# Kernel tuning notes

Hardware: AMD Instinct MI355X
Metric: run time of the kernel (lower is better)

The kernel has to match this reference:

```python
import jax, jax.numpy as jnp
import numpy as np

D_MODEL = 1024
N_HEADS = 16
D_HEAD = D_MODEL // N_HEADS
D_FF = 4096
ALPHA = 2.0
EPS = 1e-5


def _layernorm(x, g, b):
    mu = jnp.mean(x, axis=-1, keepdims=True)
    var = jnp.mean(jnp.square(x - mu), axis=-1, keepdims=True)
    return (x - mu) * jax.lax.rsqrt(var + EPS) * g + b


def _mish(x):
    return x * jnp.tanh(jax.nn.softplus(x))


def setup_inputs() -> dict:
    key = jax.random.key(0)
    ks = jax.random.split(key, 10)
    s = 1.0 / np.sqrt(D_MODEL)
    sf = 1.0 / np.sqrt(D_FF)
    return {
        "x": jax.random.normal(ks[0], (2, 2048, D_MODEL), jnp.float32),
        "Wq": jax.random.normal(ks[1], (D_MODEL, D_MODEL), jnp.float32) * s,
        "Wk": jax.random.normal(ks[2], (D_MODEL, D_MODEL), jnp.float32) * s,
        "Wv": jax.random.normal(ks[3], (D_MODEL, D_MODEL), jnp.float32) * s,
        "Wo": jax.random.normal(ks[4], (D_MODEL, D_MODEL), jnp.float32) * s,
        "W1": jax.random.normal(ks[5], (D_MODEL, D_FF), jnp.float32) * s,
        "b1": jnp.zeros((D_FF,), jnp.float32),
        "W2": jax.random.normal(ks[6], (D_FF, D_MODEL), jnp.float32) * sf,
        "b2": jnp.zeros((D_MODEL,), jnp.float32),
        "g1": jnp.ones((D_MODEL,), jnp.float32),
        "be1": jnp.zeros((D_MODEL,), jnp.float32),
        "g2": jnp.ones((D_MODEL,), jnp.float32),
        "be2": jnp.zeros((D_MODEL,), jnp.float32),
    }


def reference(x, Wq, Wk, Wv, Wo, W1, b1, W2, b2, g1, be1, g2, be2):
    B, T, C = x.shape
    # --- multi-head self-attention (no mask, eval-mode dropout) ---
    def split_heads(t):  # [B,T,C] -> [B,H,T,Dh]
        return t.reshape(B, T, N_HEADS, D_HEAD).transpose(0, 2, 1, 3)
    Q = split_heads(x @ Wq)
    K = split_heads(x @ Wk)
    V = split_heads(x @ Wv)
    scale = 1.0 / np.sqrt(D_HEAD).astype(np.float32)
    attn = jnp.einsum('bhqd,bhkd->bhqk', Q, K) * scale
    attn = jax.nn.softmax(attn, axis=-1)
    ctx = jnp.einsum('bhqk,bhkd->bhqd', attn, V)
    ctx = ctx.transpose(0, 2, 1, 3).reshape(B, T, C)
    attn_out = ctx @ Wo
    # --- DeepNorm residual 1 ---
    x = _layernorm(ALPHA * x + attn_out, g1, be1)
    # --- feed-forward (Mish) ---
    h = _mish(x @ W1 + b1)
    ff_out = h @ W2 + b2
    # --- DeepNorm residual 2 ---
    return _layernorm(ALPHA * x + ff_out, g2, be2)
```

## Files before the change

kernel.cpp:

```cpp
#include <hip/hip_runtime.h>
#include <hip/hip_bf16.h>

typedef unsigned short u16;
typedef unsigned int   u32;
typedef __attribute__((ext_vector_type(8))) short  short8;
typedef __attribute__((ext_vector_type(4))) short  short4v;
typedef __attribute__((ext_vector_type(4))) float  f32x4;

static __device__ __forceinline__ u16 f2bf(float f) {
  u32 u = __builtin_bit_cast(u32, f);
  u = (u + 0x7fffu + ((u >> 16) & 1u)) >> 16;
  return (u16)u;
}

#define MFMA_16x16x32(A,B,C) __builtin_amdgcn_mfma_f32_16x16x32_bf16((A),(B),(C),0,0,0)

static __device__ __forceinline__ void gload_lds16(const u16* g, u16* lds) {
  __builtin_amdgcn_global_load_lds((const __attribute__((address_space(1))) u32*)g,
                                   (__attribute__((address_space(3))) u32*)lds, 16, 0, 0);
}

static __device__ __forceinline__ float mishf(float x) {
  float sp = fmaxf(x, 0.f) + log1pf(__expf(-fabsf(x)));
  return x * tanhf(sp);
}

__global__ __launch_bounds__(256) void cast_bf16_kernel(const float* __restrict__ x,
                                                        u16* __restrict__ o) {
  int i = (blockIdx.x * 256 + threadIdx.x) * 4;
  float4 v = *(const float4*)&x[i];
  short4v s;
  s[0] = (short)f2bf(v.x); s[1] = (short)f2bf(v.y);
  s[2] = (short)f2bf(v.z); s[3] = (short)f2bf(v.w);
  *(short4v*)&o[i] = s;
}

__global__ __launch_bounds__(256) void transpose_cast_kernel(const float* __restrict__ W,
                                                             u16* __restrict__ Out,
                                                             int K, int N) {
  __shared__ float tile[32][33];
  const int k0 = blockIdx.y * 32, n0 = blockIdx.x * 32;
  const int tx = threadIdx.x & 31, ty = threadIdx.x >> 5;
  #pragma unroll
  for (int i = 0; i < 32; i += 8)
    tile[ty + i][tx] = W[(size_t)(k0 + ty + i) * N + n0 + tx];
  __syncthreads();
  #pragma unroll
  for (int i = 0; i < 32; i += 8)
    Out[(size_t)(n0 + ty + i) * K + k0 + tx] = f2bf(tile[tx][ty + i]);
}

template<int EPI>
__global__ __launch_bounds__(256, 2)
void gemm128(const u16* __restrict__ A, const u16* __restrict__ Bt,
             void* __restrict__ Cv, const float* __restrict__ bias,
             int M, int N, int K) {
  __shared__ __align__(16) u16 As[128 * 32];
  __shared__ __align__(16) u16 Bs[128 * 32];
  const int tid  = threadIdx.x;
  const int lane = tid & 63;
  const int wid  = tid >> 6;

  const u32 nwg = gridDim.x * gridDim.y;
  const u32 id  = blockIdx.y * gridDim.x + blockIdx.x;
  const u32 cpx = nwg >> 3;
  const u32 swz = (id & 7) * cpx + (id >> 3);
  const int bm = (swz / gridDim.x) * 128;
  const int bn = (swz % gridDim.x) * 128;

  const int wr = (wid >> 1) * 64;
  const int wc = (wid & 1) * 64;

  f32x4 acc[4][4];
  #pragma unroll
  for (int i = 0; i < 4; i++)
    #pragma unroll
    for (int j = 0; j < 4; j++) acc[i][j] = (f32x4){0.f, 0.f, 0.f, 0.f};

  const int srow = wid * 16 + (lane >> 2);
  const int scol = (lane & 3) * 8;
  const u16* Ag0 = A  + (size_t)(bm + srow) * K + scol;
  const u16* Ag1 = A  + (size_t)(bm + 64 + srow) * K + scol;
  const u16* Bg0 = Bt + (size_t)(bn + srow) * K + scol;
  const u16* Bg1 = Bt + (size_t)(bn + 64 + srow) * K + scol;
  u16* As0 = &As[wid * 512];
  u16* As1 = &As[2048 + wid * 512];
  u16* Bs0 = &Bs[wid * 512];
  u16* Bs1 = &Bs[2048 + wid * 512];

  const int fr = lane & 15;
  const int fk = (lane >> 4) * 8;

  for (int k0 = 0; k0 < K; k0 += 32) {
    gload_lds16(Ag0 + k0, As0);
    gload_lds16(Ag1 + k0, As1);
    gload_lds16(Bg0 + k0, Bs0);
    gload_lds16(Bg1 + k0, Bs1);
    __syncthreads();
    short8 af[4], bf[4];
    #pragma unroll
    for (int i = 0; i < 4; i++) af[i] = *(const short8*)&As[(wr + i * 16 + fr) * 32 + fk];
    #pragma unroll
    for (int j = 0; j < 4; j++) bf[j] = *(const short8*)&Bs[(wc + j * 16 + fr) * 32 + fk];
    #pragma unroll
    for (int i = 0; i < 4; i++)
      #pragma unroll
      for (int j = 0; j < 4; j++)
        acc[i][j] = MFMA_16x16x32(af[i], bf[j], acc[i][j]);
    __syncthreads();
  }

  const int r0 = (lane >> 4) * 4;
  #pragma unroll
  for (int i = 0; i < 4; i++) {
    const int row = bm + wr + i * 16 + r0;
    #pragma unroll
    for (int j = 0; j < 4; j++) {
      const int col = bn + wc + j * 16 + fr;
      float bv = 0.f;
      if (EPI >= 2) bv = bias[col];
      #pragma unroll
      for (int r = 0; r < 4; r++) {
        float v = acc[i][j][r] + bv;
        if (EPI == 2) v = mishf(v);
        if (EPI == 0 || EPI == 2)
          ((u16*)Cv)[(size_t)(row + r) * N + col] = f2bf(v);
        else
          ((float*)Cv)[(size_t)(row + r) * N + col] = v;
      }
    }
  }
}

__global__ __launch_bounds__(256, 2)
void attn_kernel(const u16* __restrict__ qkv, u16* __restrict__ ctx) {
  const int bh = blockIdx.y;
  const int b = bh >> 4, h = bh & 15;
  const int qt = blockIdx.x;
  const int tid = threadIdx.x, lane = tid & 63, wid = tid >> 6;

  __shared__ __align__(16) u16 Ks[32 * 72];
  __shared__ __align__(16) u16 Vt[64 * 40];
  __shared__ __align__(16) u16 Ps[4][16 * 40];

  const size_t base = (size_t)b * 2048 * 3072;
  const int fr  = lane & 15;
  const int fkb = lane >> 4;

  short8 qf[2];
  {
    const int qrow = qt * 64 + wid * 16 + fr;
    const u16* qp = qkv + base + (size_t)qrow * 3072 + h * 64 + fkb * 8;
    qf[0] = *(const short8*)qp;
    qf[1] = *(const short8*)(qp + 32);
  }

  float m_r[4], l_r[4];
  f32x4 o[4];
  #pragma unroll
  for (int r = 0; r < 4; r++) { m_r[r] = -1e30f; l_r[r] = 0.f; }
  #pragma unroll
  for (int d = 0; d < 4; d++) o[d] = (f32x4){0.f, 0.f, 0.f, 0.f};

  const int srow = tid >> 3;
  const int sd   = (tid & 7) * 8;

  for (int kt = 0; kt < 2048; kt += 32) {
    const u16* kp = qkv + base + (size_t)(kt + srow) * 3072 + 1024 + h * 64 + sd;
    short8 kv = *(const short8*)kp;
    short8 vv = *(const short8*)(kp + 1024);
    *(short8*)&Ks[srow * 72 + sd] = kv;
    const int vcol = (srow + sd) & 31;
    #pragma unroll
    for (int i = 0; i < 8; i++) Vt[(sd + i) * 40 + vcol] = (u16)vv[i];
    __syncthreads();

    f32x4 s[2];
    #pragma unroll
    for (int nb = 0; nb < 2; nb++) {
      short8 kf0 = *(const short8*)&Ks[(nb * 16 + fr) * 72 + fkb * 8];
      short8 kf1 = *(const short8*)&Ks[(nb * 16 + fr) * 72 + 32 + fkb * 8];
      f32x4 z = (f32x4){0.f, 0.f, 0.f, 0.f};
      z = MFMA_16x16x32(qf[0], kf0, z);
      z = MFMA_16x16x32(qf[1], kf1, z);
      s[nb] = z * 0.125f;
    }

    #pragma unroll
    for (int r = 0; r < 4; r++) {
      float mx = fmaxf(s[0][r], s[1][r]);
      #pragma unroll
      for (int off = 1; off < 16; off <<= 1) mx = fmaxf(mx, __shfl_xor(mx, off, 64));
      float mnew = fmaxf(m_r[r], mx);
      float corr = __expf(m_r[r] - mnew);
      float p0 = __expf(s[0][r] - mnew);
      float p1 = __expf(s[1][r] - mnew);
      float ps = p0 + p1;
      #pragma unroll
      for (int off = 1; off < 16; off <<= 1) ps += __shfl_xor(ps, off, 64);
      l_r[r] = l_r[r] * corr + ps;
      m_r[r] = mnew;
      #pragma unroll
      for (int d = 0; d < 4; d++) o[d][r] *= corr;
      s[0][r] = p0; s[1][r] = p1;
    }

    #pragma unroll
    for (int nb = 0; nb < 2; nb++)
      #pragma unroll
      for (int r = 0; r < 4; r++)
        Ps[wid][(fkb * 4 + r) * 40 + nb * 16 + fr] = f2bf(s[nb][r]);
    short8 pf = *(const short8*)&Ps[wid][fr * 40 + fkb * 8];

    #pragma unroll
    for (int db = 0; db < 4; db++) {
      short8 vf = *(const short8*)&Vt[(db * 16 + fr) * 40 + 8 * ((fkb + 2 * db + (fr >> 3)) & 3)];
      o[db] = MFMA_16x16x32(pf, vf, o[db]);
    }
    __syncthreads();
  }

  #pragma unroll
  for (int db = 0; db < 4; db++)
    #pragma unroll
    for (int r = 0; r < 4; r++) {
      float v = o[db][r] / l_r[r];
      int row = qt * 64 + wid * 16 + fkb * 4 + r;
      ctx[(size_t)(b * 2048 + row) * 1024 + h * 64 + db * 16 + fr] = f2bf(v);
    }
}

__global__ __launch_bounds__(256, 4)
void ln_kernel(const float* __restrict__ res, const float* __restrict__ add,
               const float* __restrict__ g, const float* __restrict__ be,
               float* __restrict__ yout, u16* __restrict__ ybf) {
  const int row = blockIdx.x;
  const float* rp = res + (size_t)row * 1024;
  const float* ap = add + (size_t)row * 1024;
  const int c0 = threadIdx.x * 4;
  float4 rv = *(const float4*)&rp[c0];
  float4 av = *(const float4*)&ap[c0];
  float v[4] = {2.f * rv.x + av.x, 2.f * rv.y + av.y, 2.f * rv.z + av.z, 2.f * rv.w + av.w};
  float s = 0.f, sq = 0.f;
  #pragma unroll
  for (int i = 0; i < 4; i++) { s += v[i]; sq += v[i] * v[i]; }
  #pragma unroll
  for (int off = 32; off; off >>= 1) { s += __shfl_xor(s, off, 64); sq += __shfl_xor(sq, off, 64); }
  __shared__ float red[8];
  const int wid = threadIdx.x >> 6;
  if ((threadIdx.x & 63) == 0) { red[wid] = s; red[4 + wid] = sq; }
  __syncthreads();
  s  = red[0] + red[1] + red[2] + red[3];
  sq = red[4] + red[5] + red[6] + red[7];
  const float mu   = s * (1.f / 1024.f);
  const float var  = sq * (1.f / 1024.f) - mu * mu;
  const float rstd = rsqrtf(var + 1e-5f);
  #pragma unroll
  for (int i = 0; i < 4; i++) {
    const int c = c0 + i;
    float y = (v[i] - mu) * rstd * g[c] + be[c];
    yout[(size_t)row * 1024 + c] = y;
    if (ybf) ybf[(size_t)row * 1024 + c] = f2bf(y);
  }
}

extern "C" void kernel_launch(void* const* d_in, const int* in_sizes, int n_in,
                              void* d_out, int out_size, void* d_ws, size_t ws_size,
                              hipStream_t stream) {
  const float* x   = (const float*)d_in[0];
  const float* Wq  = (const float*)d_in[1];
  const float* Wk  = (const float*)d_in[2];
  const float* Wv  = (const float*)d_in[3];
  const float* Wo  = (const float*)d_in[4];
  const float* W1  = (const float*)d_in[5];
  const float* b1  = (const float*)d_in[6];
  const float* W2  = (const float*)d_in[7];
  const float* b2  = (const float*)d_in[8];
  const float* g1  = (const float*)d_in[9];
  const float* be1 = (const float*)d_in[10];
  const float* g2  = (const float*)d_in[11];
  const float* be2 = (const float*)d_in[12];
  float* out = (float*)d_out;
  char* ws = (char*)d_ws;
  const size_t MB = 1024 * 1024;

  u16*   qkv   = (u16*)(ws + 0);
  float* y1    = (float*)(ws + 0);
  u16*   y1b   = (u16*)(ws + 16 * MB);
  u16*   hb    = (u16*)(ws + 24 * MB);
  u16*   xb    = (u16*)(ws + 24 * MB);
  u16*   WqkvT = (u16*)(ws + 32 * MB);
  u16*   WoT   = (u16*)(ws + 38 * MB);
  u16*   ctx   = (u16*)(ws + 40 * MB);
  float* attnf = (float*)(ws + 56 * MB);
  float* fff   = (float*)(ws + 56 * MB);
  u16*   W1T   = (u16*)(ws + 72 * MB);
  u16*   W2T   = (u16*)(ws + 72 * MB);

  cast_bf16_kernel<<<dim3(4096), dim3(256), 0, stream>>>(x, xb);
  transpose_cast_kernel<<<dim3(32, 32), dim3(256), 0, stream>>>(Wq, WqkvT, 1024, 1024);
  transpose_cast_kernel<<<dim3(32, 32), dim3(256), 0, stream>>>(Wk, WqkvT + 1024 * 1024, 1024, 1024);
  transpose_cast_kernel<<<dim3(32, 32), dim3(256), 0, stream>>>(Wv, WqkvT + 2 * 1024 * 1024, 1024, 1024);
  gemm128<0><<<dim3(24, 32), dim3(256), 0, stream>>>(xb, WqkvT, qkv, nullptr, 4096, 3072, 1024);
  attn_kernel<<<dim3(32, 32), dim3(256), 0, stream>>>(qkv, ctx);
  transpose_cast_kernel<<<dim3(32, 32), dim3(256), 0, stream>>>(Wo, WoT, 1024, 1024);
  gemm128<1><<<dim3(8, 32), dim3(256), 0, stream>>>(ctx, WoT, attnf, nullptr, 4096, 1024, 1024);
  ln_kernel<<<dim3(4096), dim3(256), 0, stream>>>(x, attnf, g1, be1, y1, y1b);
  transpose_cast_kernel<<<dim3(128, 32), dim3(256), 0, stream>>>(W1, W1T, 1024, 4096);
  gemm128<2><<<dim3(32, 32), dim3(256), 0, stream>>>(y1b, W1T, hb, b1, 4096, 4096, 1024);
  transpose_cast_kernel<<<dim3(32, 128), dim3(256), 0, stream>>>(W2, W2T, 4096, 1024);
  gemm128<3><<<dim3(8, 32), dim3(256), 0, stream>>>(hb, W2T, fff, b2, 4096, 1024, 4096);
  ln_kernel<<<dim3(4096), dim3(256), 0, stream>>>(y1, fff, g2, be2, out, nullptr);
}
```

Baseline: 581.5 us.

## Transpose QK^T MFMA so softmax row reductions need fewer cross-lane shuffles

The score MFMA now uses swapped operands, computing S^T, so each lane holds one query row's scores along its accumulator registers. Row max and sum then reduce mostly within registers plus two xor shuffles, replacing four-step 16-lane shuffle trees for each of four rows. P is written to LDS as packed 4-element vectors instead of scalar stores. The correction and normalizer factors are redistributed to the output layout with extra shuffles, which adds a little work per tile.

```diff
diff --git a/kernel.cpp b/kernel.cpp
--- a/kernel.cpp
+++ b/kernel.cpp
@@ -144,21 +144,19 @@
   __shared__ __align__(16) u16 Ps[4][16 * 40];
 
   const size_t base = (size_t)b * 2048 * 3072;
-  const int fr  = lane & 15;
-  const int fkb = lane >> 4;
+  const int fr = lane & 15;
+  const int g  = lane >> 4;
 
   short8 qf[2];
   {
     const int qrow = qt * 64 + wid * 16 + fr;
-    const u16* qp = qkv + base + (size_t)qrow * 3072 + h * 64 + fkb * 8;
+    const u16* qp = qkv + base + (size_t)qrow * 3072 + h * 64 + g * 8;
     qf[0] = *(const short8*)qp;
     qf[1] = *(const short8*)(qp + 32);
   }
 
-  float m_r[4], l_r[4];
+  float m_l = -1e30f, l_l = 0.f;
   f32x4 o[4];
-  #pragma unroll
-  for (int r = 0; r < 4; r++) { m_r[r] = -1e30f; l_r[r] = 0.f; }
   #pragma unroll
   for (int d = 0; d < 4; d++) o[d] = (f32x4){0.f, 0.f, 0.f, 0.f};
 
@@ -178,54 +176,71 @@
     f32x4 s[2];
     #pragma unroll
     for (int nb = 0; nb < 2; nb++) {
-      short8 kf0 = *(const short8*)&Ks[(nb * 16 + fr) * 72 + fkb * 8];
-      short8 kf1 = *(const short8*)&Ks[(nb * 16 + fr) * 72 + 32 + fkb * 8];
+      short8 kf0 = *(const short8*)&Ks[(nb * 16 + fr) * 72 + g * 8];
+      short8 kf1 = *(const short8*)&Ks[(nb * 16 + fr) * 72 + 32 + g * 8];
       f32x4 z = (f32x4){0.f, 0.f, 0.f, 0.f};
-      z = MFMA_16x16x32(qf[0], kf0, z);
-      z = MFMA_16x16x32(qf[1], kf1, z);
+      z = MFMA_16x16x32(kf0, qf[0], z);
+      z = MFMA_16x16x32(kf1, qf[1], z);
       s[nb] = z * 0.125f;
     }
 
+    float mx = s[0][0];
+    #pragma unroll
+    for (int nb = 0; nb < 2; nb++)
+      #pragma unroll
+      for (int r = 0; r < 4; r++) mx = fmaxf(mx, s[nb][r]);
+    mx = fmaxf(mx, __shfl_xor(mx, 16));
+    mx = fmaxf(mx, __shfl_xor(mx, 32));
+    const float mnew = fmaxf(m_l, mx);
+    const float corr = __expf(m_l - mnew);
+    m_l = mnew;
+    float ps = 0.f;
+    #pragma unroll
+    for (int nb = 0; nb < 2; nb++)
+      #pragma unroll
+      for (int r = 0; r < 4; r++) {
+        float e = __expf(s[nb][r] - mnew);
+        s[nb][r] = e;
+        ps += e;
+      }
+    ps += __shfl_xor(ps, 16);
+    ps += __shfl_xor(ps, 32);
+    l_l = l_l * corr + ps;
+
+    float corr_t[4];
+    #pragma unroll
+    for (int r = 0; r < 4; r++) corr_t[r] = __shfl(corr, (lane & 48) | (g * 4 + r));
+    #pragma unroll
+    for (int db = 0; db < 4; db++)
+      #pragma unroll
+      for (int r = 0; r < 4; r++) o[db][r] *= corr_t[r];
+
+    #pragma unroll
+    for (int nb = 0; nb < 2; nb++) {
+      short4v pk;
+      #pragma unroll
+      for (int r = 0; r < 4; r++) pk[r] = (short)f2bf(s[nb][r]);
+      *(short4v*)&Ps[wid][fr * 40 + nb * 16 + g * 4] = pk;
+    }
+    short8 pf = *(const short8*)&Ps[wid][fr * 40 + g * 8];
+
+    #pragma unroll
+    for (int db = 0; db < 4; db++) {
+      short8 vf = *(const short8*)&Vt[(db * 16 + fr) * 40 + 8 * ((g + 2 * db + (fr >> 3)) & 3)];
+      o[db] = MFMA_16x16x32(pf, vf, o[db]);
+    }
+    __syncthreads();
+  }
+
+  float l_t[4];
+  #pragma unroll
+  for (int r = 0; r < 4; r++) l_t[r] = __shfl(l_l, (lane & 48) | (g * 4 + r));
+  #pragma unroll
+  for (int db = 0; db < 4; db++)
     #pragma unroll
     for (int r = 0; r < 4; r++) {
-      float mx = fmaxf(s[0][r], s[1][r]);
-      #pragma unroll
-      for (int off = 1; off < 16; off <<= 1) mx = fmaxf(mx, __shfl_xor(mx, off, 64));
-      float mnew = fmaxf(m_r[r], mx);
-      float corr = __expf(m_r[r] - mnew);
-      float p0 = __expf(s[0][r] - mnew);
-      float p1 = __expf(s[1][r] - mnew);
-      float ps = p0 + p1;
-      #pragma unroll
-      for (int off = 1; off < 16; off <<= 1) ps += __shfl_xor(ps, off, 64);
-      l_r[r] = l_r[r] * corr + ps;
-      m_r[r] = mnew;
-      #pragma unroll
-      for (int d = 0; d < 4; d++) o[d][r] *= corr;
-      s[0][r] = p0; s[1][r] = p1;
-    }
-
-    #pragma unroll
-    for (int nb = 0; nb < 2; nb++)
-      #pragma unroll
-      for (int r = 0; r < 4; r++)
-        Ps[wid][(fkb * 4 + r) * 40 + nb * 16 + fr] = f2bf(s[nb][r]);
-    short8 pf = *(const short8*)&Ps[wid][fr * 40 + fkb * 8];
-
-    #pragma unroll
-    for (int db = 0; db < 4; db++) {
-      short8 vf = *(const short8*)&Vt[(db * 16 + fr) * 40 + 8 * ((fkb + 2 * db + (fr >> 3)) & 3)];
-      o[db] = MFMA_16x16x32(pf, vf, o[db]);
-    }
-    __syncthreads();
-  }
-
-  #pragma unroll
-  for (int db = 0; db < 4; db++)
-    #pragma unroll
-    for (int r = 0; r < 4; r++) {
-      float v = o[db][r] / l_r[r];
-      int row = qt * 64 + wid * 16 + fkb * 4 + r;
+      float v = o[db][r] / l_t[r];
+      int row = qt * 64 + wid * 16 + g * 4 + r;
       ctx[(size_t)(b * 2048 + row) * 1024 + h * 64 + db * 16 + fr] = f2bf(v);
     }
 }
```

After: 510.0 us. -12.3%, faster.
